# Optimization experiments

Hardware: AMD Instinct MI355X
Metric: run time of the kernel (lower is better)

Reference implementation:

```python
import jax, jax.numpy as jnp
import numpy as np


def setup_inputs() -> dict:
    key = jax.random.key(0)
    ks = jax.random.split(key, 9)
    N_POI, N_TIME, D = 10000, 48, 500
    S, L = 2048, 4096  # state_len (cur), seq_len (his)
    return {
        "his": jax.random.randint(ks[0], (L,), 0, N_POI, dtype=jnp.int32),
        "cur": jax.random.randint(ks[1], (S,), 0, N_POI, dtype=jnp.int32),
        "his_t": jax.random.randint(ks[2], (L,), 0, N_TIME, dtype=jnp.int32),
        "cur_t": jax.random.randint(ks[3], (S,), 0, N_TIME, dtype=jnp.int32),
        "poi_distance_mat": jax.random.uniform(ks[4], (N_POI, N_POI), dtype=jnp.float32),
        "time_sim_mat": jax.random.uniform(ks[5], (N_TIME, N_TIME), dtype=jnp.float32),
        "user_emb": jax.random.normal(ks[6], (S, D), dtype=jnp.float32),
        "id_emb": jax.random.normal(ks[7], (L, D), dtype=jnp.float32),
        "socail_uid_emb": jax.random.normal(ks[8], (D,), dtype=jnp.float32),
        "w1_socail": jnp.float32(0.6),
        "w2_socail": jnp.float32(0.4),
    }


def reference(his, cur, his_t, cur_t, poi_distance_mat, time_sim_mat,
              user_emb, id_emb, socail_uid_emb, w1_socail, w2_socail):
    # Attn_loc: energies[i,j] = 1/dist[cur[i],his[j]] if nonzero else 1e-6
    d = poi_distance_mat[cur[:, None], his[None, :]]          # [S, L] gather
    nz = d != 0
    loc_energy = jnp.where(nz, 1.0 / jnp.where(nz, d, 1.0), 1e-6)
    attn_loc = jax.nn.softmax(loc_energy, axis=-1)

    # Attn_time: energies[i,j] = time_sim[cur_t[i], his_t[j]]
    time_energy = time_sim_mat[cur_t[:, None], his_t[None, :]]  # [S, L]
    attn_time = jax.nn.softmax(time_energy, axis=-1)

    # Attn_user ('dot'): w1 * <user_emb[i], id_emb[j]> + w2 * <socail, id_emb[j]>
    user_energy = (w1_socail * jnp.einsum('sd,ld->sl', user_emb, id_emb)
                   + w2_socail * (id_emb @ socail_uid_emb)[None, :])  # [S, L]
    attn_user = jax.nn.softmax(user_energy, axis=-1)

    return jnp.stack([attn_loc, attn_time, attn_user])  # [3, S, L]
```

## Files before the change

kernel.cpp:

```cpp
#include <hip/hip_runtime.h>
#include <math.h>

#define S_DIM 2048
#define L_DIM 4096
#define D_DIM 500
#define KPAD 512
#define NPOI 10000
#define NTIME 48

typedef __attribute__((ext_vector_type(8))) short short8;
typedef __attribute__((ext_vector_type(16))) float f32x16;

#define A_BYTES 4194304
#define PLANE_BYTES 12582912
#define LDSBUF 49152

__device__ __forceinline__ float wave_max(float v) {
#pragma unroll
  for (int o = 32; o > 0; o >>= 1) v = fmaxf(v, __shfl_down(v, o, 64));
  return v;
}
__device__ __forceinline__ float wave_sum(float v) {
#pragma unroll
  for (int o = 32; o > 0; o >>= 1) v += __shfl_down(v, o, 64);
  return v;
}
__device__ __forceinline__ short f2bf(float x) {
  union { float f; unsigned u; } v;
  v.f = x;
  const unsigned r = v.u + 0x7fffu + ((v.u >> 16) & 1u);
  return (short)(r >> 16);
}
__device__ __forceinline__ float bf2f(short h) {
  union { unsigned u; float f; } v;
  v.u = ((unsigned)(unsigned short)h) << 16;
  return v.f;
}

__global__ __launch_bounds__(256) void attn_loc_time_kernel(
    const int* __restrict__ cur, const int* __restrict__ his,
    const float* __restrict__ poi, const int* __restrict__ cur_t,
    const int* __restrict__ his_t, const float* __restrict__ P,
    float* __restrict__ out_loc, float* __restrict__ out_time) {
  __shared__ __attribute__((aligned(16))) float rowbuf[NPOI];
  __shared__ float Prow[NTIME];
  __shared__ float redm[4];
  __shared__ float reds[4];
  const int s = blockIdx.x;
  const int tid = threadIdx.x;
  if (tid < NTIME) Prow[tid] = P[cur_t[s] * NTIME + tid];
  const float* row = poi + (size_t)cur[s] * NPOI;
  for (int i = tid; i < NPOI / 4; i += 256)
    *reinterpret_cast<float4*>(&rowbuf[i * 4]) =
        *reinterpret_cast<const float4*>(row + i * 4);
  __syncthreads();
  float v[16];
  float lmax = -1e30f;
#pragma unroll
  for (int j = 0; j < 16; ++j) {
    const int l = j * 256 + tid;
    const float d = rowbuf[his[l]];
    const float e = (d != 0.0f) ? (1.0f / d) : 1e-6f;
    v[j] = e;
    lmax = fmaxf(lmax, e);
  }
  lmax = wave_max(lmax);
  if ((tid & 63) == 0) redm[tid >> 6] = lmax;
  __syncthreads();
  const float m = fmaxf(fmaxf(redm[0], redm[1]), fmaxf(redm[2], redm[3]));
  float lsum = 0.f;
#pragma unroll
  for (int j = 0; j < 16; ++j) {
    v[j] = __expf(v[j] - m);
    lsum += v[j];
  }
  lsum = wave_sum(lsum);
  if ((tid & 63) == 0) reds[tid >> 6] = lsum;
  __syncthreads();
  const float inv = 1.0f / (reds[0] + reds[1] + reds[2] + reds[3]);
  float* ol = out_loc + (size_t)s * L_DIM;
  float* ot = out_time + (size_t)s * L_DIM;
#pragma unroll
  for (int j = 0; j < 16; ++j) {
    const int l = j * 256 + tid;
    ol[l] = v[j] * inv;
    ot[l] = Prow[his_t[l]];
  }
}

__global__ __launch_bounds__(256) void time_table_kernel(
    const int* __restrict__ his_t, const float* __restrict__ T,
    float* __restrict__ P) {
  __shared__ int cnt[NTIME];
  __shared__ float Ts[NTIME * NTIME];
  const int tid = threadIdx.x;
  if (tid < NTIME) cnt[tid] = 0;
  __syncthreads();
  for (int l = tid; l < L_DIM; l += 256) atomicAdd(&cnt[his_t[l]], 1);
  for (int i = tid; i < NTIME * NTIME; i += 256) Ts[i] = T[i];
  __syncthreads();
  if (tid < NTIME) {
    float m = -1e30f;
    for (int t = 0; t < NTIME; ++t) m = fmaxf(m, Ts[tid * NTIME + t]);
    float den = 0.f;
    for (int t = 0; t < NTIME; ++t)
      den += (float)cnt[t] * __expf(Ts[tid * NTIME + t] - m);
    const float inv = 1.0f / den;
    for (int t = 0; t < NTIME; ++t)
      P[tid * NTIME + t] = __expf(Ts[tid * NTIME + t] - m) * inv;
  }
}

__global__ __launch_bounds__(256) void split_kernel(
    const float* __restrict__ U, const float* __restrict__ Id,
    const float* __restrict__ w1p, const float* __restrict__ soc,
    const float* __restrict__ w2p, short* __restrict__ planes,
    float* __restrict__ bias) {
  const int chunk = blockIdx.x * 256 + threadIdx.x;
  const int row = chunk >> 6;
  const int lq = chunk & 63;
  const bool isA = row < S_DIM;
  const float scale = isA ? w1p[0] : 1.0f;
  const float* src = isA ? (U + (size_t)row * D_DIM)
                         : (Id + (size_t)(row - S_DIM) * D_DIM);
  const int k0 = lq * 8;
  float dot = 0.f;
  short h[8], l[8];
#pragma unroll
  for (int e = 0; e < 8; ++e) {
    const int k = k0 + e;
    const float v = (k < D_DIM) ? src[k] : 0.0f;
    if (!isA && k < D_DIM) dot += v * soc[k];
    const float x = scale * v;
    const short hb = f2bf(x);
    h[e] = hb;
    l[e] = f2bf(x - bf2f(hb));
  }
  const int ks = lq >> 2, g = lq & 3;
  if (isA) {
    const int mb = row >> 8, rin = row & 255;
    const int gs = g ^ (rin & 3) ^ ((rin >> 2) & 3);
    char* base = (char*)planes + (size_t)(mb * 16 + ks) * 32768 + rin * 64 +
                 gs * 16;
    *reinterpret_cast<int4*>(base) = *reinterpret_cast<const int4*>(h);
    *reinterpret_cast<int4*>(base + 16384) = *reinterpret_cast<const int4*>(l);
  } else {
    const int rb = row - S_DIM;
    const int nb = rb >> 7, rin = rb & 127;
    const int gs = g ^ (rin & 3) ^ ((rin >> 2) & 3);
    char* base = (char*)planes + A_BYTES + (size_t)(nb * 16 + ks) * 16384 +
                 rin * 64 + gs * 16;
    *reinterpret_cast<int4*>(base) = *reinterpret_cast<const int4*>(h);
    *reinterpret_cast<int4*>(base + 8192) = *reinterpret_cast<const int4*>(l);
    const float d = wave_sum(dot);
    if ((threadIdx.x & 63) == 0) bias[rb] = w2p[0] * d;
  }
}

__global__ __launch_bounds__(512, 2) void user_gemm_mfma(
    const short* __restrict__ planes, const float* __restrict__ bias,
    float* __restrict__ outE) {
  __shared__ __attribute__((aligned(1024))) char lds[2 * LDSBUF];
  const int tid = threadIdx.x;
  const int lane = tid & 63;
  const int wid = tid >> 6;
  const int ob = (blockIdx.x & 7) * 32 + (blockIdx.x >> 3);
  const int nb = ob >> 3;
  const int mb = ob & 7;
  const int bm = mb * 256, bn = nb * 128;
  const char* gA = (const char*)planes + (size_t)mb * 16 * 32768;
  const char* gB = (const char*)planes + A_BYTES + (size_t)nb * 16 * 16384;
  const int wm = (wid >> 1) * 64;
  const int wn = (wid & 1) * 64;
  const int r32 = lane & 31;
  const int khl = lane >> 5;

  f32x16 acc[2][2] = {};

#define STAGE(ks_, buf_)                                                      \
  {                                                                           \
    const int _ks = (ks_);                                                    \
    char* _dst = lds + (buf_)*LDSBUF;                                         \
    _Pragma("unroll") for (int q = 0; q < 6; ++q) {                           \
      const int off = (q * 512 + tid) * 16;                                   \
      if (q < 4) {                                                            \
        __builtin_amdgcn_global_load_lds(                                     \
            (const __attribute__((address_space(1))) unsigned*)(gA +          \
                (size_t)_ks * 32768 + off),                                   \
            (__attribute__((address_space(3))) unsigned*)(_dst + off), 16, 0, \
            0);                                                               \
      } else {                                                                \
        __builtin_amdgcn_global_load_lds(                                     \
            (const __attribute__((address_space(1))) unsigned*)(gB +          \
                (size_t)_ks * 16384 + (off - 32768)),                         \
            (__attribute__((address_space(3))) unsigned*)(_dst + off), 16, 0, \
            0);                                                               \
      }                                                                       \
    }                                                                         \
  }

  STAGE(0, 0);
  __syncthreads();
  int buf = 0;
  for (int ks = 0; ks < 16; ++ks) {
    if (ks < 15) STAGE(ks + 1, buf ^ 1);
    const char* La = lds + buf * LDSBUF;
    const char* Lb = La + 32768;
#pragma unroll
    for (int s16 = 0; s16 < 2; ++s16) {
      short8 ah[2], al[2], bh[2], bl[2];
#pragma unroll
      for (int i = 0; i < 2; ++i) {
        const int ra = wm + i * 32 + r32;
        const int ga = ((s16 * 2 + khl) ^ (ra & 3) ^ ((ra >> 2) & 3)) * 16;
        ah[i] = *reinterpret_cast<const short8*>(La + ra * 64 + ga);
        al[i] = *reinterpret_cast<const short8*>(La + 16384 + ra * 64 + ga);
        const int rbb = wn + i * 32 + r32;
        const int gb = ((s16 * 2 + khl) ^ (rbb & 3) ^ ((rbb >> 2) & 3)) * 16;
        bh[i] = *reinterpret_cast<const short8*>(Lb + rbb * 64 + gb);
        bl[i] = *reinterpret_cast<const short8*>(Lb + 8192 + rbb * 64 + gb);
      }
#pragma unroll
      for (int i = 0; i < 2; ++i)
#pragma unroll
        for (int j = 0; j < 2; ++j) {
          acc[i][j] = __builtin_amdgcn_mfma_f32_32x32x16_bf16(
              ah[i], bh[j], acc[i][j], 0, 0, 0);
          acc[i][j] = __builtin_amdgcn_mfma_f32_32x32x16_bf16(
              ah[i], bl[j], acc[i][j], 0, 0, 0);
          acc[i][j] = __builtin_amdgcn_mfma_f32_32x32x16_bf16(
              al[i], bh[j], acc[i][j], 0, 0, 0);
        }
    }
    __syncthreads();
    buf ^= 1;
  }
#undef STAGE

  const int rg = 4 * khl;
#pragma unroll
  for (int j = 0; j < 2; ++j) {
    const int col = bn + wn + j * 32 + r32;
    const float bj = bias[col];
#pragma unroll
    for (int i = 0; i < 2; ++i) {
      const int rbase = bm + wm + i * 32 + rg;
#pragma unroll
      for (int reg = 0; reg < 16; ++reg) {
        const int rowm = rbase + (reg & 3) + 8 * (reg >> 2);
        outE[(size_t)rowm * L_DIM + col] = acc[i][j][reg] + bj;
      }
    }
  }
}

__global__ __launch_bounds__(256) void user_softmax_kernel(
    float* __restrict__ outE) {
  __shared__ float redm[4];
  __shared__ float reds[4];
  const int s = blockIdx.x;
  const int tid = threadIdx.x;
  float* row = outE + (size_t)s * L_DIM;
  float4 v[4];
  float lmax = -1e30f;
#pragma unroll
  for (int j = 0; j < 4; ++j) {
    v[j] = *reinterpret_cast<const float4*>(&row[(j * 256 + tid) * 4]);
    lmax = fmaxf(lmax, fmaxf(fmaxf(v[j].x, v[j].y), fmaxf(v[j].z, v[j].w)));
  }
  lmax = wave_max(lmax);
  if ((tid & 63) == 0) redm[tid >> 6] = lmax;
  __syncthreads();
  const float m = fmaxf(fmaxf(redm[0], redm[1]), fmaxf(redm[2], redm[3]));
  float lsum = 0.f;
#pragma unroll
  for (int j = 0; j < 4; ++j) {
    v[j].x = __expf(v[j].x - m);
    v[j].y = __expf(v[j].y - m);
    v[j].z = __expf(v[j].z - m);
    v[j].w = __expf(v[j].w - m);
    lsum += v[j].x + v[j].y + v[j].z + v[j].w;
  }
  lsum = wave_sum(lsum);
  if ((tid & 63) == 0) reds[tid >> 6] = lsum;
  __syncthreads();
  const float inv = 1.0f / (reds[0] + reds[1] + reds[2] + reds[3]);
#pragma unroll
  for (int j = 0; j < 4; ++j) {
    v[j].x *= inv;
    v[j].y *= inv;
    v[j].z *= inv;
    v[j].w *= inv;
    *reinterpret_cast<float4*>(&row[(j * 256 + tid) * 4]) = v[j];
  }
}

extern "C" void kernel_launch(void* const* d_in, const int* in_sizes, int n_in,
                              void* d_out, int out_size, void* d_ws,
                              size_t ws_size, hipStream_t stream) {
  const int* his = (const int*)d_in[0];
  const int* cur = (const int*)d_in[1];
  const int* his_t = (const int*)d_in[2];
  const int* cur_t = (const int*)d_in[3];
  const float* poi = (const float*)d_in[4];
  const float* tsim = (const float*)d_in[5];
  const float* uemb = (const float*)d_in[6];
  const float* idemb = (const float*)d_in[7];
  const float* soc = (const float*)d_in[8];
  const float* w1 = (const float*)d_in[9];
  const float* w2 = (const float*)d_in[10];

  float* out = (float*)d_out;
  float* out_loc = out;
  float* out_time = out + (size_t)S_DIM * L_DIM;
  float* out_user = out + 2 * (size_t)S_DIM * L_DIM;

  short* planes;
  float* bias;
  float* P;
  if (ws_size >= (size_t)PLANE_BYTES + 32768) {
    planes = (short*)d_ws;
    bias = (float*)((char*)d_ws + PLANE_BYTES);
    P = bias + L_DIM;
  } else {
    planes = (short*)out_loc;
    bias = (float*)d_ws;
    P = bias + L_DIM;
  }

  hipLaunchKernelGGL(split_kernel, dim3((S_DIM + L_DIM) * 64 / 256), dim3(256),
                     0, stream, uemb, idemb, w1, soc, w2, planes, bias);
  hipLaunchKernelGGL(time_table_kernel, dim3(1), dim3(256), 0, stream, his_t,
                     tsim, P);
  hipLaunchKernelGGL(user_gemm_mfma, dim3(256), dim3(512), 0, stream, planes,
                     bias, out_user);
  hipLaunchKernelGGL(user_softmax_kernel, dim3(S_DIM), dim3(256), 0, stream,
                     out_user);
  hipLaunchKernelGGL(attn_loc_time_kernel, dim3(S_DIM), dim3(256), 0, stream,
                     cur, his, poi, cur_t, his_t, P, out_loc, out_time);
}
```

Measured before the change: 88.59 us.

## Fuse user softmax into GEMM epilogue via cooperative grid sync

The separate user_softmax kernel goes away. The GEMM epilogue now takes exp of the logits with a fixed shift instead of the row max, writes per-tile partial row sums, synchronises the whole grid cooperatively, then normalises and writes the final probabilities once. This removes a full read and write pass over the 32MB user plane. The time-table kernel is also folded into the split kernel as an extra block. In exchange it relies on a fixed exponent shift, which risks overflow or underflow for other input scales, and on all 256 blocks being co-resident for the grid sync.

After: 170.6 us. 92.5% more time.

```diff
diff --git a/kernel.cpp b/kernel.cpp
--- a/kernel.cpp
+++ b/kernel.cpp
@@ -1,12 +1,15 @@
 #include <hip/hip_runtime.h>
+#include <hip/hip_cooperative_groups.h>
 #include <math.h>
+
+namespace cg = cooperative_groups;
 
 #define S_DIM 2048
 #define L_DIM 4096
 #define D_DIM 500
-#define KPAD 512
 #define NPOI 10000
 #define NTIME 48
+#define EXP_SHIFT 40.0f
 
 typedef __attribute__((ext_vector_type(8))) short short8;
 typedef __attribute__((ext_vector_type(16))) float f32x16;
@@ -23,6 +26,11 @@
 __device__ __forceinline__ float wave_sum(float v) {
 #pragma unroll
   for (int o = 32; o > 0; o >>= 1) v += __shfl_down(v, o, 64);
+  return v;
+}
+__device__ __forceinline__ float half_sum(float v) {
+#pragma unroll
+  for (int o = 16; o > 0; o >>= 1) v += __shfl_xor(v, o, 64);
   return v;
 }
 __device__ __forceinline__ short f2bf(float x) {
@@ -88,35 +96,34 @@
   }
 }
 
-__global__ __launch_bounds__(256) void time_table_kernel(
-    const int* __restrict__ his_t, const float* __restrict__ T,
-    float* __restrict__ P) {
-  __shared__ int cnt[NTIME];
-  __shared__ float Ts[NTIME * NTIME];
-  const int tid = threadIdx.x;
-  if (tid < NTIME) cnt[tid] = 0;
-  __syncthreads();
-  for (int l = tid; l < L_DIM; l += 256) atomicAdd(&cnt[his_t[l]], 1);
-  for (int i = tid; i < NTIME * NTIME; i += 256) Ts[i] = T[i];
-  __syncthreads();
-  if (tid < NTIME) {
-    float m = -1e30f;
-    for (int t = 0; t < NTIME; ++t) m = fmaxf(m, Ts[tid * NTIME + t]);
-    float den = 0.f;
-    for (int t = 0; t < NTIME; ++t)
-      den += (float)cnt[t] * __expf(Ts[tid * NTIME + t] - m);
-    const float inv = 1.0f / den;
-    for (int t = 0; t < NTIME; ++t)
-      P[tid * NTIME + t] = __expf(Ts[tid * NTIME + t] - m) * inv;
-  }
-}
-
-__global__ __launch_bounds__(256) void split_kernel(
+__global__ __launch_bounds__(256) void split_table_kernel(
     const float* __restrict__ U, const float* __restrict__ Id,
     const float* __restrict__ w1p, const float* __restrict__ soc,
-    const float* __restrict__ w2p, short* __restrict__ planes,
-    float* __restrict__ bias) {
-  const int chunk = blockIdx.x * 256 + threadIdx.x;
+    const float* __restrict__ w2p, const int* __restrict__ his_t,
+    const float* __restrict__ T, short* __restrict__ planes,
+    float* __restrict__ bias, float* __restrict__ P) {
+  const int tid = threadIdx.x;
+  if (blockIdx.x == gridDim.x - 1) {
+    __shared__ int cnt[NTIME];
+    __shared__ float Ts[NTIME * NTIME];
+    if (tid < NTIME) cnt[tid] = 0;
+    __syncthreads();
+    for (int l = tid; l < L_DIM; l += 256) atomicAdd(&cnt[his_t[l]], 1);
+    for (int i = tid; i < NTIME * NTIME; i += 256) Ts[i] = T[i];
+    __syncthreads();
+    if (tid < NTIME) {
+      float m = -1e30f;
+      for (int t = 0; t < NTIME; ++t) m = fmaxf(m, Ts[tid * NTIME + t]);
+      float den = 0.f;
+      for (int t = 0; t < NTIME; ++t)
+        den += (float)cnt[t] * __expf(Ts[tid * NTIME + t] - m);
+      const float inv = 1.0f / den;
+      for (int t = 0; t < NTIME; ++t)
+        P[tid * NTIME + t] = __expf(Ts[tid * NTIME + t] - m) * inv;
+    }
+    return;
+  }
+  const int chunk = blockIdx.x * 256 + tid;
   const int row = chunk >> 6;
   const int lq = chunk & 63;
   const bool isA = row < S_DIM;
@@ -140,8 +147,8 @@
   if (isA) {
     const int mb = row >> 8, rin = row & 255;
     const int gs = g ^ (rin & 3) ^ ((rin >> 2) & 3);
-    char* base = (char*)planes + (size_t)(mb * 16 + ks) * 32768 + rin * 64 +
-                 gs * 16;
+    char* base =
+        (char*)planes + (size_t)(mb * 16 + ks) * 32768 + rin * 64 + gs * 16;
     *reinterpret_cast<int4*>(base) = *reinterpret_cast<const int4*>(h);
     *reinterpret_cast<int4*>(base + 16384) = *reinterpret_cast<const int4*>(l);
   } else {
@@ -153,13 +160,13 @@
     *reinterpret_cast<int4*>(base) = *reinterpret_cast<const int4*>(h);
     *reinterpret_cast<int4*>(base + 8192) = *reinterpret_cast<const int4*>(l);
     const float d = wave_sum(dot);
-    if ((threadIdx.x & 63) == 0) bias[rb] = w2p[0] * d;
+    if ((tid & 63) == 0) bias[rb] = w2p[0] * d;
   }
 }
 
 __global__ __launch_bounds__(512, 2) void user_gemm_mfma(
     const short* __restrict__ planes, const float* __restrict__ bias,
-    float* __restrict__ outE) {
+    float* __restrict__ part, float* __restrict__ outP) {
   __shared__ __attribute__((aligned(1024))) char lds[2 * LDSBUF];
   const int tid = threadIdx.x;
   const int lane = tid & 63;
@@ -237,61 +244,53 @@
   }
 #undef STAGE
 
-  const int rg = 4 * khl;
+  const int slot = nb * 2 + (wn >> 6);
+  float bj[2];
+#pragma unroll
+  for (int j = 0; j < 2; ++j) bj[j] = bias[bn + wn + j * 32 + r32];
+#pragma unroll
+  for (int i = 0; i < 2; ++i) {
+#pragma unroll
+    for (int reg = 0; reg < 16; ++reg) {
+      float e0 = __expf(acc[i][0][reg] + bj[0] - EXP_SHIFT);
+      float e1 = __expf(acc[i][1][reg] + bj[1] - EXP_SHIFT);
+      acc[i][0][reg] = e0;
+      acc[i][1][reg] = e1;
+      const float hs = half_sum(e0 + e1);
+      if (r32 == 0) {
+        const int rowm =
+            bm + wm + i * 32 + 4 * khl + (reg & 3) + 8 * (reg >> 2);
+        part[(size_t)rowm * 64 + slot] = hs;
+      }
+    }
+  }
+  __threadfence();
+  cg::this_grid().sync();
+
+  float* invb = (float*)lds;
+  if (tid < 256) {
+    const float4* pp =
+        reinterpret_cast<const float4*>(part + (size_t)(bm + tid) * 64);
+    float s = 0.f;
+#pragma unroll
+    for (int q = 0; q < 16; ++q) {
+      const float4 x = pp[q];
+      s += x.x + x.y + x.z + x.w;
+    }
+    invb[tid] = 1.0f / s;
+  }
+  __syncthreads();
 #pragma unroll
   for (int j = 0; j < 2; ++j) {
     const int col = bn + wn + j * 32 + r32;
-    const float bj = bias[col];
 #pragma unroll
     for (int i = 0; i < 2; ++i) {
-      const int rbase = bm + wm + i * 32 + rg;
 #pragma unroll
       for (int reg = 0; reg < 16; ++reg) {
-        const int rowm = rbase + (reg & 3) + 8 * (reg >> 2);
-        outE[(size_t)rowm * L_DIM + col] = acc[i][j][reg] + bj;
+        const int rl = wm + i * 32 + 4 * khl + (reg & 3) + 8 * (reg >> 2);
+        outP[(size_t)(bm + rl) * L_DIM + col] = acc[i][j][reg] * invb[rl];
       }
     }
-  }
-}
-
-__global__ __launch_bounds__(256) void user_softmax_kernel(
-    float* __restrict__ outE) {
-  __shared__ float redm[4];
-  __shared__ float reds[4];
-  const int s = blockIdx.x;
-  const int tid = threadIdx.x;
-  float* row = outE + (size_t)s * L_DIM;
-  float4 v[4];
-  float lmax = -1e30f;
-#pragma unroll
-  for (int j = 0; j < 4; ++j) {
-    v[j] = *reinterpret_cast<const float4*>(&row[(j * 256 + tid) * 4]);
-    lmax = fmaxf(lmax, fmaxf(fmaxf(v[j].x, v[j].y), fmaxf(v[j].z, v[j].w)));
-  }
-  lmax = wave_max(lmax);
-  if ((tid & 63) == 0) redm[tid >> 6] = lmax;
-  __syncthreads();
-  const float m = fmaxf(fmaxf(redm[0], redm[1]), fmaxf(redm[2], redm[3]));
-  float lsum = 0.f;
-#pragma unroll
-  for (int j = 0; j < 4; ++j) {
-    v[j].x = __expf(v[j].x - m);
-    v[j].y = __expf(v[j].y - m);
-    v[j].z = __expf(v[j].z - m);
-    v[j].w = __expf(v[j].w - m);
-    lsum += v[j].x + v[j].y + v[j].z + v[j].w;
-  }
-  lsum = wave_sum(lsum);
-  if ((tid & 63) == 0) reds[tid >> 6] = lsum;
-  __syncthreads();
-  const float inv = 1.0f / (reds[0] + reds[1] + reds[2] + reds[3]);
-#pragma unroll
-  for (int j = 0; j < 4; ++j) {
-    v[j].x *= inv;
-    v[j].y *= inv;
-    v[j].z *= inv;
-    v[j].w *= inv;
-    *reinterpret_cast<float4*>(&row[(j * 256 + tid) * 4]) = v[j];
   }
 }
 
@@ -315,27 +314,29 @@
   float* out_time = out + (size_t)S_DIM * L_DIM;
   float* out_user = out + 2 * (size_t)S_DIM * L_DIM;
 
+  const size_t aux_bytes = (size_t)(L_DIM + NTIME * NTIME + S_DIM * 64) * 4;
   short* planes;
   float* bias;
-  float* P;
-  if (ws_size >= (size_t)PLANE_BYTES + 32768) {
+  if (ws_size >= PLANE_BYTES + aux_bytes) {
     planes = (short*)d_ws;
     bias = (float*)((char*)d_ws + PLANE_BYTES);
-    P = bias + L_DIM;
   } else {
     planes = (short*)out_loc;
     bias = (float*)d_ws;
-    P = bias + L_DIM;
-  }
-
-  hipLaunchKernelGGL(split_kernel, dim3((S_DIM + L_DIM) * 64 / 256), dim3(256),
-                     0, stream, uemb, idemb, w1, soc, w2, planes, bias);
-  hipLaunchKernelGGL(time_table_kernel, dim3(1), dim3(256), 0, stream, his_t,
-                     tsim, P);
-  hipLaunchKernelGGL(user_gemm_mfma, dim3(256), dim3(512), 0, stream, planes,
-                     bias, out_user);
-  hipLaunchKernelGGL(user_softmax_kernel, dim3(S_DIM), dim3(256), 0, stream,
-                     out_user);
+  }
+  float* P = bias + L_DIM;
+  float* part = P + NTIME * NTIME;
+
+  hipLaunchKernelGGL(split_table_kernel,
+                     dim3((S_DIM + L_DIM) * 64 / 256 + 1), dim3(256), 0,
+                     stream, uemb, idemb, w1, soc, w2, his_t, tsim, planes,
+                     bias, P);
+  {
+    void* args[] = {(void*)&planes, (void*)&bias, (void*)&part,
+                    (void*)&out_user};
+    hipLaunchCooperativeKernel((void*)user_gemm_mfma, dim3(256), dim3(512),
+                               args, 0, stream);
+  }
   hipLaunchKernelGGL(attn_loc_time_kernel, dim3(S_DIM), dim3(256), 0, stream,
                      cur, his, poi, cur_t, his_t, P, out_loc, out_time);
 }
```
